# Optimization experiments

Measured on AMD Instinct MI355X. Metric: run time of the kernel, lower is better.

Reference implementation:

```python
import jax, jax.numpy as jnp
import numpy as np

B, SQ, SK, D, H = 8, 1024, 1024, 768, 12
HD = D // H  # 64


def setup_inputs() -> dict:
    key = jax.random.key(0)
    ks = jax.random.split(key, 6)
    s = 0.02
    return {
        "hidden_states": jax.random.normal(ks[0], (B, SQ, D), jnp.float32),
        "context": jax.random.normal(ks[1], (B, SK, D), jnp.float32),
        "attention_mask": jnp.zeros((B, 1, 1, SK), jnp.float32),
        "Wq": jax.random.normal(ks[2], (D, D), jnp.float32) * s,
        "bq": jnp.zeros((D,), jnp.float32),
        "Wk": jax.random.normal(ks[3], (D, D), jnp.float32) * s,
        "bk": jnp.zeros((D,), jnp.float32),
        "Wv": jax.random.normal(ks[4], (D, D), jnp.float32) * s,
        "bv": jnp.zeros((D,), jnp.float32),
    }


def _split_heads(x):
    # [B, S, D] -> [B, H, S, HD]
    b, s, _ = x.shape
    return x.reshape(b, s, H, HD).transpose(0, 2, 1, 3)


def reference(hidden_states, context, attention_mask, Wq, bq, Wk, bk, Wv, bv):
    q = _split_heads(hidden_states @ Wq + bq)   # [B,H,SQ,HD]
    k = _split_heads(context @ Wk + bk)         # [B,H,SK,HD]
    v = _split_heads(context @ Wv + bv)         # [B,H,SK,HD]
    scores = jnp.einsum("bhqd,bhkd->bhqk", q, k) / jnp.sqrt(jnp.float32(HD))
    scores = scores + attention_mask            # broadcast [B,1,1,SK]
    probs = jax.nn.softmax(scores, axis=-1)     # dropout p=0 -> identity
    ctx = jnp.einsum("bhqk,bhkd->bhqd", probs, v)
    return ctx.transpose(0, 2, 1, 3).reshape(hidden_states.shape[0], -1, H * HD)
```

## Files before the change

### kernel.cpp

```cpp
#include <hip/hip_runtime.h>
#include <hip/hip_bf16.h>
#include <cstdint>

#define B_  8
#define SQ_ 1024
#define SK_ 1024
#define D_  768
#define H_  12
#define HD_ 64

typedef __attribute__((ext_vector_type(8))) short s16x8;
typedef __attribute__((ext_vector_type(4))) float f32x4;

__device__ __forceinline__ float bf2f(ushort u) {
    union { uint32_t i; float f; } v; v.i = ((uint32_t)u) << 16; return v.f;
}
__device__ __forceinline__ ushort f2bf(float f) {
    __hip_bfloat16 h = __float2bfloat16(f);
    union { __hip_bfloat16 h; ushort u; } v; v.h = h; return v.u;
}

__global__ void convX(const float4* __restrict__ src, ushort* __restrict__ dst, int n4) {
    int i = blockIdx.x * blockDim.x + threadIdx.x;
    int stride = gridDim.x * blockDim.x;
    for (; i < n4; i += stride) {
        float4 v = src[i];
        ushort4 o = { f2bf(v.x), f2bf(v.y), f2bf(v.z), f2bf(v.w) };
        *reinterpret_cast<ushort4*>(dst + (size_t)i * 4) = o;
    }
}

__global__ void convWT(const float* __restrict__ W, ushort* __restrict__ WT) {
    __shared__ float t[32][33];
    int k0 = blockIdx.x * 32, n0 = blockIdx.y * 32;
    int tx = threadIdx.x & 31, ty = threadIdx.x >> 5;
#pragma unroll
    for (int rr = 0; rr < 4; ++rr)
        t[ty + 8 * rr][tx] = W[(size_t)(k0 + ty + 8 * rr) * D_ + n0 + tx];
    __syncthreads();
#pragma unroll
    for (int rr = 0; rr < 4; ++rr)
        WT[(size_t)(n0 + ty + 8 * rr) * D_ + k0 + tx] = f2bf(t[tx][ty + 8 * rr]);
}

#define GL16(g, l)                                                                     \
    __builtin_amdgcn_global_load_lds((const __attribute__((address_space(1))) void*)(g), \
                                     (__attribute__((address_space(3))) void*)(l), 16, 0, 0)

__global__ __launch_bounds__(256) void gemm_qkv(
    const ushort* __restrict__ hb, const ushort* __restrict__ cb,
    const ushort* __restrict__ wqt, const ushort* __restrict__ wkt, const ushort* __restrict__ wvt,
    const float* __restrict__ bq, const float* __restrict__ bk, const float* __restrict__ bv,
    ushort* __restrict__ qout, ushort* __restrict__ kout, ushort* __restrict__ vtout)
{
    const int z = blockIdx.z;
    const ushort* A    = (z == 0) ? hb : cb;
    const ushort* Wt   = (z == 0) ? wqt : (z == 1) ? wkt : wvt;
    const float*  bias = (z == 0) ? bq  : (z == 1) ? bk  : bv;

    __shared__ ushort As[128 * 32];
    __shared__ ushort Bs[128 * 32];

    const int tid = threadIdx.x;
    const int w = tid >> 6, l = tid & 63;
    const int g = l >> 4, c = l & 15;
    const int wr = w >> 1, wc = w & 1;
    const int m0 = blockIdx.x * 128;
    const int n0 = blockIdx.y * 128;

    f32x4 acc[4][4];
#pragma unroll
    for (int mi = 0; mi < 4; ++mi)
#pragma unroll
        for (int ni = 0; ni < 4; ++ni) acc[mi][ni] = (f32x4){0.f, 0.f, 0.f, 0.f};

    for (int kt = 0; kt < D_ / 32; ++kt) {
        __syncthreads();
#pragma unroll
        for (int j = 0; j < 2; ++j) {
            int cc = (j * 4 + w) * 64 + l;
            int row = cc >> 2, c8 = cc & 3;
            const ushort* ga = A  + (size_t)(m0 + row) * D_ + kt * 32 + c8 * 8;
            GL16(ga, (char*)As + (size_t)(j * 4 + w) * 1024);
            const ushort* gb = Wt + (size_t)(n0 + row) * D_ + kt * 32 + c8 * 8;
            GL16(gb, (char*)Bs + (size_t)(j * 4 + w) * 1024);
        }
        __syncthreads();

        s16x8 af[4], bfr[4];
#pragma unroll
        for (int mi = 0; mi < 4; ++mi)
            af[mi] = *(const s16x8*)&As[(wr * 64 + mi * 16 + c) * 32 + g * 8];
#pragma unroll
        for (int ni = 0; ni < 4; ++ni)
            bfr[ni] = *(const s16x8*)&Bs[(wc * 64 + ni * 16 + c) * 32 + g * 8];
#pragma unroll
        for (int mi = 0; mi < 4; ++mi)
#pragma unroll
            for (int ni = 0; ni < 4; ++ni)
                acc[mi][ni] = __builtin_amdgcn_mfma_f32_16x16x32_bf16(af[mi], bfr[ni], acc[mi][ni], 0, 0, 0);
    }

    if (z < 2) {
        ushort* Out = (z == 0) ? qout : kout;
#pragma unroll
        for (int ni = 0; ni < 4; ++ni) {
            int ncol = n0 + wc * 64 + ni * 16 + c;
            float bv_ = bias[ncol];
#pragma unroll
            for (int mi = 0; mi < 4; ++mi) {
#pragma unroll
                for (int r = 0; r < 4; ++r) {
                    int mrow = m0 + wr * 64 + mi * 16 + 4 * g + r;
                    Out[(size_t)mrow * D_ + ncol] = f2bf(acc[mi][ni][r] + bv_);
                }
            }
        }
    } else {
#pragma unroll
        for (int ni = 0; ni < 4; ++ni) {
            int ncol = n0 + wc * 64 + ni * 16 + c;
            float bv_ = bias[ncol];
            int hh = ncol >> 6, dd = ncol & 63;
#pragma unroll
            for (int mi = 0; mi < 4; ++mi) {
                int mrow = m0 + wr * 64 + mi * 16 + 4 * g;
                int bb = mrow >> 10, ss = mrow & 1023;
                ushort4 pk;
                pk.x = f2bf(acc[mi][ni][0] + bv_);
                pk.y = f2bf(acc[mi][ni][1] + bv_);
                pk.z = f2bf(acc[mi][ni][2] + bv_);
                pk.w = f2bf(acc[mi][ni][3] + bv_);
                *reinterpret_cast<ushort4*>(vtout + (size_t)((bb * H_ + hh) * HD_ + dd) * SK_ + ss) = pk;
            }
        }
    }
}

__global__ __launch_bounds__(256) void attn(
    const ushort* __restrict__ Qb, const ushort* __restrict__ Kb, const ushort* __restrict__ VT,
    const float* __restrict__ amask, float* __restrict__ out)
{
    __shared__ ushort Ks[64 * 64];
    __shared__ ushort Vs[64 * 64];
    __shared__ ushort Ps[4][16 * 64];

    const int tid = threadIdx.x;
    const int w = tid >> 6, l = tid & 63;
    const int g = l >> 4, c = l & 15;
    const int q0 = blockIdx.x * 64;
    const int h  = blockIdx.y;
    const int b  = blockIdx.z;

    s16x8 qf[2];
#pragma unroll
    for (int kk = 0; kk < 2; ++kk) {
        const ushort* gq = Qb + (size_t)(b * SQ_ + q0 + w * 16 + c) * D_ + h * HD_ + kk * 32 + g * 8;
        s16x8 v = *(const s16x8*)gq;
#pragma unroll
        for (int i = 0; i < 8; ++i) v[i] = (short)f2bf(bf2f((ushort)v[i]) * 0.125f);
        qf[kk] = v;
    }

    f32x4 o[4];
#pragma unroll
    for (int nn = 0; nn < 4; ++nn) o[nn] = (f32x4){0.f, 0.f, 0.f, 0.f};
    float m_run[4], ps[4];
#pragma unroll
    for (int r = 0; r < 4; ++r) { m_run[r] = -INFINITY; ps[r] = 0.f; }

    const float L2E = 1.44269504f;

    for (int t = 0; t < SK_ / 64; ++t) {
        const int kv0 = t * 64;
        __syncthreads();
#pragma unroll
        for (int j = 0; j < 2; ++j) {
            int cc = j * 256 + tid;
            int row = cc >> 3, c8 = cc & 7;
            int ldsb = row * 128 + ((c8 * 16) ^ ((row & 7) << 4));
            uint4 kv_ = *(const uint4*)(Kb + (size_t)(b * SK_ + kv0 + row) * D_ + h * HD_ + c8 * 8);
            *(uint4*)((char*)Ks + ldsb) = kv_;
            uint4 vv_ = *(const uint4*)(VT + (size_t)((b * H_ + h) * HD_ + row) * SK_ + kv0 + c8 * 8);
            *(uint4*)((char*)Vs + ldsb) = vv_;
        }
        __syncthreads();

        float sv[4][4];
#pragma unroll
        for (int n = 0; n < 4; ++n) {
            f32x4 s = (f32x4){0.f, 0.f, 0.f, 0.f};
#pragma unroll
            for (int kk = 0; kk < 2; ++kk) {
                const s16x8 bf_ = *(const s16x8*)((const char*)Ks + (16 * n + c) * 128 +
                                                  ((kk * 64 + g * 16) ^ ((c & 7) << 4)));
                s = __builtin_amdgcn_mfma_f32_16x16x32_bf16(qf[kk], bf_, s, 0, 0, 0);
            }
            float mv = amask[b * SK_ + kv0 + 16 * n + c];
#pragma unroll
            for (int r = 0; r < 4; ++r) sv[n][r] = s[r] + mv;
        }

        float pmax[4];
#pragma unroll
        for (int r = 0; r < 4; ++r)
            pmax[r] = fmaxf(fmaxf(sv[0][r], sv[1][r]), fmaxf(sv[2][r], sv[3][r]));
        int ok = 1;
#pragma unroll
        for (int r = 0; r < 4; ++r) ok &= (pmax[r] <= m_run[r] + 8.f);
        if (!__all(ok)) {
            float alpha[4];
#pragma unroll
            for (int r = 0; r < 4; ++r) {
                float m_ = pmax[r];
                m_ = fmaxf(m_, __shfl_xor(m_, 1));
                m_ = fmaxf(m_, __shfl_xor(m_, 2));
                m_ = fmaxf(m_, __shfl_xor(m_, 4));
                m_ = fmaxf(m_, __shfl_xor(m_, 8));
                float mn = fmaxf(m_run[r], m_);
                alpha[r] = exp2f((m_run[r] - mn) * L2E);
                m_run[r] = mn;
                ps[r] *= alpha[r];
            }
#pragma unroll
            for (int nn = 0; nn < 4; ++nn)
#pragma unroll
                for (int r = 0; r < 4; ++r) o[nn][r] *= alpha[r];
        }
#pragma unroll
        for (int n = 0; n < 4; ++n)
#pragma unroll
            for (int r = 0; r < 4; ++r) {
                float p = exp2f((sv[n][r] - m_run[r]) * L2E);
                sv[n][r] = p;
                ps[r] += p;
            }

#pragma unroll
        for (int n = 0; n < 4; ++n)
#pragma unroll
            for (int r = 0; r < 4; ++r) {
                int row = 4 * g + r;
                *(ushort*)((char*)&Ps[w][0] + row * 128 +
                           (((16 * n + c) * 2) ^ ((row & 7) << 4))) = f2bf(sv[n][r]);
            }
        s16x8 pa[2];
#pragma unroll
        for (int kk = 0; kk < 2; ++kk)
            pa[kk] = *(const s16x8*)((const char*)&Ps[w][0] + c * 128 +
                                     ((kk * 64 + g * 16) ^ ((c & 7) << 4)));
#pragma unroll
        for (int nn = 0; nn < 4; ++nn) {
#pragma unroll
            for (int kk = 0; kk < 2; ++kk) {
                const s16x8 bv_ = *(const s16x8*)((const char*)Vs + (16 * nn + c) * 128 +
                                                  ((kk * 64 + g * 16) ^ ((c & 7) << 4)));
                o[nn] = __builtin_amdgcn_mfma_f32_16x16x32_bf16(pa[kk], bv_, o[nn], 0, 0, 0);
            }
        }
    }

    float inv[4];
#pragma unroll
    for (int r = 0; r < 4; ++r) {
        float s_ = ps[r];
        s_ += __shfl_xor(s_, 1);
        s_ += __shfl_xor(s_, 2);
        s_ += __shfl_xor(s_, 4);
        s_ += __shfl_xor(s_, 8);
        inv[r] = 1.f / s_;
    }
#pragma unroll
    for (int nn = 0; nn < 4; ++nn)
#pragma unroll
        for (int r = 0; r < 4; ++r)
            out[(size_t)(b * SQ_ + q0 + w * 16 + 4 * g + r) * D_ + h * HD_ + 16 * nn + c] =
                o[nn][r] * inv[r];
}

extern "C" void kernel_launch(void* const* d_in, const int* in_sizes, int n_in,
                              void* d_out, int out_size, void* d_ws, size_t ws_size,
                              hipStream_t stream) {
    (void)in_sizes; (void)n_in; (void)out_size; (void)ws_size;
    const float* hidden  = (const float*)d_in[0];
    const float* context = (const float*)d_in[1];
    const float* amask   = (const float*)d_in[2];
    const float* Wq = (const float*)d_in[3];
    const float* bq = (const float*)d_in[4];
    const float* Wk = (const float*)d_in[5];
    const float* bk = (const float*)d_in[6];
    const float* Wv = (const float*)d_in[7];
    const float* bv = (const float*)d_in[8];
    float* out = (float*)d_out;

    char* ws = (char*)d_ws;
    ushort* hb  = (ushort*)(ws);
    ushort* cb  = (ushort*)(ws + 12582912);
    ushort* wqt = (ushort*)(ws + 25165824);
    ushort* wkt = (ushort*)(ws + 26345472);
    ushort* wvt = (ushort*)(ws + 27525120);
    ushort* qb  = (ushort*)(ws + 28704768);
    ushort* kb  = (ushort*)(ws + 41287680);
    ushort* vt  = (ushort*)(ws + 53870592);

    int n4 = (B_ * SQ_ * D_) / 4;
    convX<<<2048, 256, 0, stream>>>((const float4*)hidden, hb, n4);
    convX<<<2048, 256, 0, stream>>>((const float4*)context, cb, n4);
    dim3 gw(24, 24);
    convWT<<<gw, 256, 0, stream>>>(Wq, wqt);
    convWT<<<gw, 256, 0, stream>>>(Wk, wkt);
    convWT<<<gw, 256, 0, stream>>>(Wv, wvt);
    gemm_qkv<<<dim3(64, 6, 3), 256, 0, stream>>>(hb, cb, wqt, wkt, wvt, bq, bk, bv, qb, kb, vt);
    attn<<<dim3(16, 12, 8), 256, 0, stream>>>(qb, kb, vt, amask, out);
}
```

Baseline: 238.1 us.

## Double-buffer K/V tiles and compute transposed scores to keep P in registers

Rewrites the attention inner loop to double-buffer K and V tiles in LDS, issuing the global loads for the next tile before computing on the current one and using a single barrier per tile. The QK^T MFMA operands are swapped so each lane owns a full query column, which lets the softmax max and sum reduce with two cross-row shuffles instead of four per row. P is rearranged into the PV A-operand through lane shuffles rather than a round trip through LDS. The attention mask is staged once into shared memory. This costs twice the K/V LDS footprint, more registers for the prefetched tiles, and many shuffle instructions per tile.

```diff
diff --git a/kernel.cpp b/kernel.cpp
--- a/kernel.cpp
+++ b/kernel.cpp
@@ -18,6 +18,9 @@
 __device__ __forceinline__ ushort f2bf(float f) {
     __hip_bfloat16 h = __float2bfloat16(f);
     union { __hip_bfloat16 h; ushort u; } v; v.h = h; return v.u;
+}
+__device__ __forceinline__ uint32_t pk32(float a, float b) {
+    return (uint32_t)f2bf(a) | ((uint32_t)f2bf(b) << 16);
 }
 
 __global__ void convX(const float4* __restrict__ src, ushort* __restrict__ dst, int n4) {
@@ -141,9 +144,9 @@
     const ushort* __restrict__ Qb, const ushort* __restrict__ Kb, const ushort* __restrict__ VT,
     const float* __restrict__ amask, float* __restrict__ out)
 {
-    __shared__ ushort Ks[64 * 64];
-    __shared__ ushort Vs[64 * 64];
-    __shared__ ushort Ps[4][16 * 64];
+    __shared__ ushort Ks[2][64 * 64];
+    __shared__ ushort Vs[2][64 * 64];
+    __shared__ float  Ms[1024];
 
     const int tid = threadIdx.x;
     const int w = tid >> 6, l = tid & 63;
@@ -151,6 +154,14 @@
     const int q0 = blockIdx.x * 64;
     const int h  = blockIdx.y;
     const int b  = blockIdx.z;
+    const int xsw = (c & 7) << 4;
+    const int lane0 = c + 16 * ((2 * g) & 3);
+    const int lane1 = c + 16 * ((2 * g + 1) & 3);
+    const bool hi_ = (g >= 2);
+    const float L2E = 1.44269504f;
+
+#pragma unroll
+    for (int i = 0; i < 4; ++i) Ms[tid + 256 * i] = amask[b * SK_ + tid + 256 * i];
 
     s16x8 qf[2];
 #pragma unroll
@@ -162,120 +173,135 @@
         qf[kk] = v;
     }
 
+    const int row0 = tid >> 3, c8 = tid & 7;
+    const int ldsoff = row0 * 128 + ((c8 * 16) ^ ((row0 & 7) << 4));
+    const ushort* kp = Kb + (size_t)(b * SK_ + row0) * D_ + h * HD_ + c8 * 8;
+    const ushort* vp = VT + (size_t)((b * H_ + h) * HD_ + row0) * SK_ + c8 * 8;
+
+    {
+        uint4 k0 = *(const uint4*)kp, k1 = *(const uint4*)(kp + 32 * D_);
+        uint4 v0 = *(const uint4*)vp, v1 = *(const uint4*)(vp + 32 * SK_);
+        *(uint4*)((char*)Ks[0] + ldsoff) = k0;
+        *(uint4*)((char*)Ks[0] + ldsoff + 4096) = k1;
+        *(uint4*)((char*)Vs[0] + ldsoff) = v0;
+        *(uint4*)((char*)Vs[0] + ldsoff + 4096) = v1;
+        kp += 64 * D_; vp += 64;
+    }
+    __syncthreads();
+
     f32x4 o[4];
 #pragma unroll
     for (int nn = 0; nn < 4; ++nn) o[nn] = (f32x4){0.f, 0.f, 0.f, 0.f};
-    float m_run[4], ps[4];
-#pragma unroll
-    for (int r = 0; r < 4; ++r) { m_run[r] = -INFINITY; ps[r] = 0.f; }
-
-    const float L2E = 1.44269504f;
-
-    for (int t = 0; t < SK_ / 64; ++t) {
-        const int kv0 = t * 64;
-        __syncthreads();
-#pragma unroll
-        for (int j = 0; j < 2; ++j) {
-            int cc = j * 256 + tid;
-            int row = cc >> 3, c8 = cc & 7;
-            int ldsb = row * 128 + ((c8 * 16) ^ ((row & 7) << 4));
-            uint4 kv_ = *(const uint4*)(Kb + (size_t)(b * SK_ + kv0 + row) * D_ + h * HD_ + c8 * 8);
-            *(uint4*)((char*)Ks + ldsb) = kv_;
-            uint4 vv_ = *(const uint4*)(VT + (size_t)((b * H_ + h) * HD_ + row) * SK_ + kv0 + c8 * 8);
-            *(uint4*)((char*)Vs + ldsb) = vv_;
-        }
-        __syncthreads();
-
-        float sv[4][4];
-#pragma unroll
-        for (int n = 0; n < 4; ++n) {
-            f32x4 s = (f32x4){0.f, 0.f, 0.f, 0.f};
-#pragma unroll
-            for (int kk = 0; kk < 2; ++kk) {
-                const s16x8 bf_ = *(const s16x8*)((const char*)Ks + (16 * n + c) * 128 +
-                                                  ((kk * 64 + g * 16) ^ ((c & 7) << 4)));
-                s = __builtin_amdgcn_mfma_f32_16x16x32_bf16(qf[kk], bf_, s, 0, 0, 0);
-            }
-            float mv = amask[b * SK_ + kv0 + 16 * n + c];
-#pragma unroll
-            for (int r = 0; r < 4; ++r) sv[n][r] = s[r] + mv;
-        }
-
-        float pmax[4];
-#pragma unroll
-        for (int r = 0; r < 4; ++r)
-            pmax[r] = fmaxf(fmaxf(sv[0][r], sv[1][r]), fmaxf(sv[2][r], sv[3][r]));
-        int ok = 1;
-#pragma unroll
-        for (int r = 0; r < 4; ++r) ok &= (pmax[r] <= m_run[r] + 8.f);
-        if (!__all(ok)) {
-            float alpha[4];
-#pragma unroll
-            for (int r = 0; r < 4; ++r) {
-                float m_ = pmax[r];
-                m_ = fmaxf(m_, __shfl_xor(m_, 1));
-                m_ = fmaxf(m_, __shfl_xor(m_, 2));
-                m_ = fmaxf(m_, __shfl_xor(m_, 4));
-                m_ = fmaxf(m_, __shfl_xor(m_, 8));
-                float mn = fmaxf(m_run[r], m_);
-                alpha[r] = exp2f((m_run[r] - mn) * L2E);
-                m_run[r] = mn;
-                ps[r] *= alpha[r];
-            }
-#pragma unroll
-            for (int nn = 0; nn < 4; ++nn)
-#pragma unroll
-                for (int r = 0; r < 4; ++r) o[nn][r] *= alpha[r];
-        }
-#pragma unroll
-        for (int n = 0; n < 4; ++n)
-#pragma unroll
-            for (int r = 0; r < 4; ++r) {
-                float p = exp2f((sv[n][r] - m_run[r]) * L2E);
-                sv[n][r] = p;
-                ps[r] += p;
-            }
-
-#pragma unroll
-        for (int n = 0; n < 4; ++n)
-#pragma unroll
-            for (int r = 0; r < 4; ++r) {
-                int row = 4 * g + r;
-                *(ushort*)((char*)&Ps[w][0] + row * 128 +
-                           (((16 * n + c) * 2) ^ ((row & 7) << 4))) = f2bf(sv[n][r]);
-            }
-        s16x8 pa[2];
-#pragma unroll
-        for (int kk = 0; kk < 2; ++kk)
-            pa[kk] = *(const s16x8*)((const char*)&Ps[w][0] + c * 128 +
-                                     ((kk * 64 + g * 16) ^ ((c & 7) << 4)));
-#pragma unroll
-        for (int nn = 0; nn < 4; ++nn) {
-#pragma unroll
-            for (int kk = 0; kk < 2; ++kk) {
-                const s16x8 bv_ = *(const s16x8*)((const char*)Vs + (16 * nn + c) * 128 +
-                                                  ((kk * 64 + g * 16) ^ ((c & 7) << 4)));
-                o[nn] = __builtin_amdgcn_mfma_f32_16x16x32_bf16(pa[kk], bv_, o[nn], 0, 0, 0);
-            }
-        }
-    }
-
-    float inv[4];
-#pragma unroll
-    for (int r = 0; r < 4; ++r) {
-        float s_ = ps[r];
-        s_ += __shfl_xor(s_, 1);
-        s_ += __shfl_xor(s_, 2);
-        s_ += __shfl_xor(s_, 4);
-        s_ += __shfl_xor(s_, 8);
-        inv[r] = 1.f / s_;
-    }
-#pragma unroll
-    for (int nn = 0; nn < 4; ++nn)
-#pragma unroll
-        for (int r = 0; r < 4; ++r)
-            out[(size_t)(b * SQ_ + q0 + w * 16 + 4 * g + r) * D_ + h * HD_ + 16 * nn + c] =
-                o[nn][r] * inv[r];
+    float m_run = -INFINITY, ps = 0.f;
+
+#define TILE(CUR, NXT, T)                                                              \
+    {                                                                                  \
+                                 \
+        uint4 nk0 = *(const uint4*)kp;                                                 \
+        uint4 nk1 = *(const uint4*)(kp + 32 * D_);                                     \
+        uint4 nv0 = *(const uint4*)vp;                                                 \
+        uint4 nv1 = *(const uint4*)(vp + 32 * SK_);                                    \
+        if ((T) < 14) { kp += 64 * D_; vp += 64; }                                     \
+                             \
+        float sv[4][4];                                                                \
+        _Pragma("unroll")                                                              \
+        for (int n = 0; n < 4; ++n) {                                                  \
+            f32x4 s = (f32x4){0.f, 0.f, 0.f, 0.f};                                     \
+            _Pragma("unroll")                                                          \
+            for (int kk = 0; kk < 2; ++kk) {                                           \
+                const s16x8 kf = *(const s16x8*)((const char*)Ks[CUR] +                \
+                    (16 * n + c) * 128 + ((kk * 64 + g * 16) ^ xsw));                  \
+                s = __builtin_amdgcn_mfma_f32_16x16x32_bf16(kf, qf[kk], s, 0, 0, 0);   \
+            }                                                                          \
+            const f32x4 mk = *(const f32x4*)&Ms[(T) * 64 + n * 16 + g * 4];            \
+            _Pragma("unroll")                                                          \
+            for (int r = 0; r < 4; ++r) sv[n][r] = s[r] + mk[r];                       \
+        }                                                                              \
+                                     \
+        float pmax = sv[0][0];                                                         \
+        _Pragma("unroll")                                                              \
+        for (int n = 0; n < 4; ++n)                                                    \
+            _Pragma("unroll")                                                          \
+            for (int r = 0; r < 4; ++r) pmax = fmaxf(pmax, sv[n][r]);                  \
+        if (__any(pmax > m_run + 8.f)) {                                               \
+            float mf = fmaxf(pmax, __shfl_xor(pmax, 16));                              \
+            mf = fmaxf(mf, __shfl_xor(mf, 32));                                        \
+            float mn = fmaxf(m_run, mf);                                               \
+            float alpha = exp2f((m_run - mn) * L2E);                                   \
+            m_run = mn; ps *= alpha;                                                   \
+            float ar0 = __shfl(alpha, 4 * g), ar1 = __shfl(alpha, 4 * g + 1);          \
+            float ar2 = __shfl(alpha, 4 * g + 2), ar3 = __shfl(alpha, 4 * g + 3);      \
+            _Pragma("unroll")                                                          \
+            for (int nn = 0; nn < 4; ++nn) {                                           \
+                o[nn][0] *= ar0; o[nn][1] *= ar1; o[nn][2] *= ar2; o[nn][3] *= ar3;    \
+            }                                                                          \
+        }                                                                              \
+                                          \
+        uint32_t pk[4][2];                                                             \
+        _Pragma("unroll")                                                              \
+        for (int n = 0; n < 4; ++n) {                                                  \
+            float p0 = exp2f((sv[n][0] - m_run) * L2E);                                \
+            float p1 = exp2f((sv[n][1] - m_run) * L2E);                                \
+            float p2 = exp2f((sv[n][2] - m_run) * L2E);                                \
+            float p3 = exp2f((sv[n][3] - m_run) * L2E);                                \
+            ps += (p0 + p1) + (p2 + p3);                                               \
+            pk[n][0] = pk32(p0, p1); pk[n][1] = pk32(p2, p3);                          \
+        }                                                                              \
+         \
+        s16x8 pa0, pa1;                                                                \
+        {                                                                              \
+            union { uint32_t u[4]; s16x8 v; } ua, ub;                                  \
+            uint32_t a0 = __shfl((int)pk[0][0], lane0), b0 = __shfl((int)pk[1][0], lane0); \
+            uint32_t a1 = __shfl((int)pk[0][1], lane0), b1 = __shfl((int)pk[1][1], lane0); \
+            uint32_t a2 = __shfl((int)pk[0][0], lane1), b2 = __shfl((int)pk[1][0], lane1); \
+            uint32_t a3 = __shfl((int)pk[0][1], lane1), b3 = __shfl((int)pk[1][1], lane1); \
+            ua.u[0] = hi_ ? b0 : a0; ua.u[1] = hi_ ? b1 : a1;                          \
+            ua.u[2] = hi_ ? b2 : a2; ua.u[3] = hi_ ? b3 : a3;                          \
+            uint32_t c0 = __shfl((int)pk[2][0], lane0), d0 = __shfl((int)pk[3][0], lane0); \
+            uint32_t c1 = __shfl((int)pk[2][1], lane0), d1 = __shfl((int)pk[3][1], lane0); \
+            uint32_t c2 = __shfl((int)pk[2][0], lane1), d2 = __shfl((int)pk[3][0], lane1); \
+            uint32_t c3 = __shfl((int)pk[2][1], lane1), d3 = __shfl((int)pk[3][1], lane1); \
+            ub.u[0] = hi_ ? d0 : c0; ub.u[1] = hi_ ? d1 : c1;                          \
+            ub.u[2] = hi_ ? d2 : c2; ub.u[3] = hi_ ? d3 : c3;                          \
+            pa0 = ua.v; pa1 = ub.v;                                                    \
+        }                                                                              \
+                                                                       \
+        _Pragma("unroll")                                                              \
+        for (int nn = 0; nn < 4; ++nn) {                                               \
+            const s16x8 vf0 = *(const s16x8*)((const char*)Vs[CUR] +                   \
+                (16 * nn + c) * 128 + ((g * 16) ^ xsw));                               \
+            o[nn] = __builtin_amdgcn_mfma_f32_16x16x32_bf16(pa0, vf0, o[nn], 0, 0, 0); \
+            const s16x8 vf1 = *(const s16x8*)((const char*)Vs[CUR] +                   \
+                (16 * nn + c) * 128 + ((64 + g * 16) ^ xsw));                          \
+            o[nn] = __builtin_amdgcn_mfma_f32_16x16x32_bf16(pa1, vf1, o[nn], 0, 0, 0); \
+        }                                                                              \
+                       \
+        *(uint4*)((char*)Ks[NXT] + ldsoff) = nk0;                                      \
+        *(uint4*)((char*)Ks[NXT] + ldsoff + 4096) = nk1;                               \
+        *(uint4*)((char*)Vs[NXT] + ldsoff) = nv0;                                      \
+        *(uint4*)((char*)Vs[NXT] + ldsoff + 4096) = nv1;                               \
+        __syncthreads();                                                               \
+    }
+
+    for (int tt = 0; tt < 8; ++tt) {
+        TILE(0, 1, 2 * tt)
+        TILE(1, 0, 2 * tt + 1)
+    }
+#undef TILE
+
+    ps += __shfl_xor(ps, 16);
+    ps += __shfl_xor(ps, 32);
+    float invc = 1.f / ps;
+    float ir0 = __shfl(invc, 4 * g), ir1 = __shfl(invc, 4 * g + 1);
+    float ir2 = __shfl(invc, 4 * g + 2), ir3 = __shfl(invc, 4 * g + 3);
+#pragma unroll
+    for (int nn = 0; nn < 4; ++nn) {
+        float* op = out + (size_t)(b * SQ_ + q0 + w * 16 + 4 * g) * D_ + h * HD_ + 16 * nn + c;
+        op[0]      = o[nn][0] * ir0;
+        op[D_]     = o[nn][1] * ir1;
+        op[2 * D_] = o[nn][2] * ir2;
+        op[3 * D_] = o[nn][3] * ir3;
+    }
 }
 
 extern "C" void kernel_launch(void* const* d_in, const int* in_sizes, int n_in,
```

After: 237.2 us. Within noise of the previous version (-0.3%).
